# Performance work log

Hardware: AMD Instinct MI355X
Metric: run time of the kernel (lower is better)

## Reference

```python
import jax, jax.numpy as jnp
import numpy as np

N_BASE = 4          # len('NACGT'[1:])
STATE_LEN = 5
S = N_BASE ** STATE_LEN   # 1024 states
NZ = N_BASE + 1           # 5 transitions per state
T_STEPS = 800
BATCH = 32


def _build_idx():
    # idx[i] = [i, 0*256 + i//4, 1*256 + i//4, 2*256 + i//4, 3*256 + i//4]
    i = np.arange(S)
    trans = np.stack([j * (S // N_BASE) + i // N_BASE for j in range(N_BASE)], axis=1)
    idx = np.concatenate([i[:, None], trans], axis=1).astype(np.int64)      # (S, NZ)
    # transposed transition structure (stable sort: duplicates grouped deterministically)
    idx_T = np.argsort(idx.ravel(), kind='stable').reshape(S, NZ)
    idx_T_div = idx_T // NZ
    return jnp.asarray(idx), jnp.asarray(idx_T), jnp.asarray(idx_T_div)


def _scan(Ms, idx, v0):
    """Log-semiring recurrence: alpha[t+1] = logsumexp(Ms[t] + alpha[t][:, idx], -1).
    Ms: (T, N, S, NZ); idx: (S, NZ); v0: (N, S). Returns (T+1, N, S)."""
    def step(alpha, M):
        nxt = jax.scipy.special.logsumexp(M + alpha[:, idx], axis=-1)  # (N, S)
        return nxt, nxt
    _, alphas = jax.lax.scan(step, v0, Ms)
    return jnp.concatenate([v0[None], alphas], axis=0)


def setup_inputs() -> dict:
    key = jax.random.key(0)
    scores = jax.random.normal(key, (T_STEPS, BATCH, S * NZ), dtype=jnp.float32)
    return {"scores": scores}


def reference(scores):
    idx, idx_T, idx_T_div = _build_idx()
    T, N, _ = scores.shape
    Ms = scores.reshape(T, N, S, NZ)
    v0 = jnp.zeros((N, S), scores.dtype)   # semiring Log.one == 0.0
    # forward scores
    fwd = _scan(Ms, idx, v0)                                   # (T+1, N, S)
    # backward scores: gather transposed transitions, run scan in reverse time
    Ms_T = scores[:, :, idx_T]                                 # (T, N, S, NZ)
    bwd = jnp.flip(_scan(jnp.flip(Ms_T, 0), idx_T_div, v0), 0)  # (T+1, N, S)
    posts = jax.nn.softmax(fwd + bwd, axis=-1)                 # (T+1, N, S)
    return (jnp.swapaxes(scores, 0, 1),
            jnp.swapaxes(bwd, 0, 1),
            jnp.swapaxes(posts, 0, 1))
```

## Files before the change

### kernel.cpp

```cpp
#include <hip/hip_runtime.h>

#define T_STEPS 800
#define NBATCH  32
#define SST     1024
#define ROW     5120
#define STRIDE  (NBATCH * ROW)
#define NSLOT   4

__device__ __forceinline__ float lse5(float v0, float v1, float v2, float v3, float v4) {
  float m = fmaxf(fmaxf(fmaxf(v0, v1), fmaxf(v2, v3)), v4);
  float s = __expf(v0 - m) + __expf(v1 - m) + __expf(v2 - m) +
            __expf(v3 - m) + __expf(v4 - m);
  return m + __logf(s);
}

#define WAITVM(N) do { \
  asm volatile("s_waitcnt vmcnt(" #N ")" ::: "memory"); \
  __builtin_amdgcn_sched_barrier(0); } while (0)

__device__ __forceinline__ void barrier_lgkm() {
  asm volatile("s_waitcnt lgkmcnt(0)" ::: "memory");
  __builtin_amdgcn_s_barrier();
  asm volatile("" ::: "memory");
}

template <int DIR>
__device__ void loader_run(const float* __restrict__ base,
                           float* __restrict__ out0n, int l, int lane,
                           float* __restrict__ ring) {
  const int loff = 1280 * l + 4 * lane;
  const ptrdiff_t str = DIR ? -(ptrdiff_t)STRIDE : (ptrdiff_t)STRIDE;
  const float* gIss = base + (size_t)(DIR ? (T_STEPS - 1) * STRIDE : 0) + loff;
  float* ringl = ring + loff;

  float4 A0, A1, A2, A3, A4, B0, B1, B2, B3, B4, C0, C1, C2, C3, C4;

#define LOADSET(R0,R1,R2,R3,R4) do { \
    const float4* gp_ = (const float4*)gIss; \
    R0 = gp_[0]; R1 = gp_[64]; R2 = gp_[128]; R3 = gp_[192]; R4 = gp_[256]; \
    gIss += str; } while (0)

#define WRITESET(R0,R1,R2,R3,R4) do { \
    float4* lw_ = (float4*)lsWr; \
    lw_[0] = R0; lw_[64] = R1; lw_[128] = R2; lw_[192] = R3; lw_[256] = R4; \
    if constexpr (!DIR) { \
      float4* op_ = (float4*)oSt; \
      op_[0] = R0; op_[64] = R1; op_[128] = R2; op_[192] = R3; op_[256] = R4; \
      oSt += ROW; } \
    wslot = (wslot + 1) & (NSLOT - 1); \
    lsWr = ringl + wslot * ROW; } while (0)

  LOADSET(A0,A1,A2,A3,A4);
  LOADSET(B0,B1,B2,B3,B4);
  LOADSET(C0,C1,C2,C3,C4);
  int wslot = 0;
  float* lsWr = ringl;
  float* oSt = out0n + loff;
  WAITVM(10);
  WRITESET(A0,A1,A2,A3,A4);
  if constexpr (!DIR) { WAITVM(10); } else { WAITVM(5); }
  WRITESET(B0,B1,B2,B3,B4);
  barrier_lgkm();

#define LSTEP(I0,I1,I2,I3,I4, W0,W1,W2,W3,W4) do { \
    LOADSET(I0,I1,I2,I3,I4); \
    if constexpr (!DIR) { WAITVM(10); } else { WAITVM(5); } \
    WRITESET(W0,W1,W2,W3,W4); \
    barrier_lgkm(); } while (0)

  for (int c = 0; c < 265; ++c) {
    LSTEP(A0,A1,A2,A3,A4, C0,C1,C2,C3,C4);
    LSTEP(B0,B1,B2,B3,B4, A0,A1,A2,A3,A4);
    LSTEP(C0,C1,C2,C3,C4, B0,B1,B2,B3,B4);
  }
  LSTEP(A0,A1,A2,A3,A4, C0,C1,C2,C3,C4);
  LSTEP(B0,B1,B2,B3,B4, A0,A1,A2,A3,A4);
  if constexpr (!DIR) { WAITVM(5); } else { WAITVM(0); }
  WRITESET(B0,B1,B2,B3,B4);
  barrier_lgkm();
  barrier_lgkm();
  barrier_lgkm();
#undef LSTEP
#undef WRITESET
#undef LOADSET
}

template <int DIR>
__device__ void compute_run(float* __restrict__ out, int n, int u,
                            const float* __restrict__ ring, float (*abuf)[SST]) {
  float* outn = out + (size_t)n * (T_STEPS + 1) * SST;
  float a[4] = {0.f, 0.f, 0.f, 0.f};

  {
    const float4 z = {0.f, 0.f, 0.f, 0.f};
    *(float4*)&abuf[0][4 * u] = z;
    const size_t t0 = DIR ? (size_t)T_STEPS : 0;
    ((float4*)(outn + t0 * SST))[u] = z;
  }
  barrier_lgkm();

  const float* rb = ring;
  int slot = 0;
  for (int s = 0; s < T_STEPS; ++s) {
    const int cur = s & 1, nxt = cur ^ 1;
    const float4* rv = (const float4*)(rb + 20 * u);
    const float4 q0 = rv[0], q1 = rv[1], q2 = rv[2], q3 = rv[3], q4 = rv[4];
    float fv[20];
    fv[0]=q0.x; fv[1]=q0.y; fv[2]=q0.z; fv[3]=q0.w;
    fv[4]=q1.x; fv[5]=q1.y; fv[6]=q1.z; fv[7]=q1.w;
    fv[8]=q2.x; fv[9]=q2.y; fv[10]=q2.z; fv[11]=q2.w;
    fv[12]=q3.x; fv[13]=q3.y; fv[14]=q3.z; fv[15]=q3.w;
    fv[16]=q4.x; fv[17]=q4.y; fv[18]=q4.z; fv[19]=q4.w;

    float na[4];
    if constexpr (!DIR) {
      const int q = u >> 2;
      const float p0 = abuf[cur][q];
      const float p1 = abuf[cur][q + 256];
      const float p2 = abuf[cur][q + 512];
      const float p3 = abuf[cur][q + 768];
#pragma unroll
      for (int j = 0; j < 4; ++j) {
        na[j] = lse5(fv[5*j] + a[j], fv[5*j+1] + p0, fv[5*j+2] + p1,
                     fv[5*j+3] + p2, fv[5*j+4] + p3);
        a[j] = na[j];
      }
      const float4 o = {na[0], na[1], na[2], na[3]};
      ((float4*)(outn + (size_t)(s + 1) * SST))[u] = o;
      *(float4*)&abuf[nxt][4 * u] = o;
    } else {
      const float4 pv = *(const float4*)&abuf[cur][4 * u];
      const float s0 = rb[5*u], s1 = rb[5*u+1280], s2 = rb[5*u+2560], s3 = rb[5*u+3840];
      const int t = T_STEPS - 1 - s;
      na[0] = lse5(s0 + a[0], fv[1] + pv.x, fv[6] + pv.y, fv[11] + pv.z, fv[16] + pv.w);
      na[1] = lse5(s1 + a[1], fv[2] + pv.x, fv[7] + pv.y, fv[12] + pv.z, fv[17] + pv.w);
      na[2] = lse5(s2 + a[2], fv[3] + pv.x, fv[8] + pv.y, fv[13] + pv.z, fv[18] + pv.w);
      na[3] = lse5(s3 + a[3], fv[4] + pv.x, fv[9] + pv.y, fv[14] + pv.z, fv[19] + pv.w);
#pragma unroll
      for (int j = 0; j < 4; ++j) {
        a[j] = na[j];
        outn[(size_t)t * SST + u + 256 * j] = na[j];
        abuf[nxt][u + 256 * j] = na[j];
      }
    }
    barrier_lgkm();
    slot = (slot + 1) & (NSLOT - 1);
    rb = ring + slot * ROW;
  }
}

__global__ __launch_bounds__(512, 1) void mega(const float* __restrict__ scores,
                                               float* __restrict__ out0,
                                               float* __restrict__ bwdo,
                                               float* __restrict__ fposts) {
  __shared__ float ring[NSLOT * ROW];
  __shared__ float abuf[2][SST];
  const int b = blockIdx.x;
  const int tid = threadIdx.x;
  const int n = (b < NBATCH) ? b : (b - NBATCH);
  const float* base = scores + (size_t)n * ROW;

  if (b < NBATCH) {
    if (tid < 256) compute_run<0>(fposts, n, tid, ring, abuf);
    else loader_run<0>(base, out0 + (size_t)n * T_STEPS * ROW,
                       (tid >> 6) - 4, tid & 63, ring);
  } else {
    if (tid < 256) compute_run<1>(bwdo, n, tid, ring, abuf);
    else loader_run<1>(base, nullptr, (tid >> 6) - 4, tid & 63, ring);
  }
}

__global__ __launch_bounds__(256) void posts_kernel(float* __restrict__ fp,
                                                    const float* __restrict__ bp) {
  const int lane = threadIdx.x & 63;
  const int wid  = threadIdx.x >> 6;
  const size_t row = (size_t)blockIdx.x * 4 + wid;
  float* f = fp + row * SST;
  const float* b = bp + row * SST;

  float x[16];
#pragma unroll
  for (int k = 0; k < 4; ++k) {
    const float4 fv = ((const float4*)f)[lane + 64 * k];
    const float4 bv = ((const float4*)b)[lane + 64 * k];
    x[4 * k + 0] = fv.x + bv.x;
    x[4 * k + 1] = fv.y + bv.y;
    x[4 * k + 2] = fv.z + bv.z;
    x[4 * k + 3] = fv.w + bv.w;
  }
  float m = x[0];
#pragma unroll
  for (int j = 1; j < 16; ++j) m = fmaxf(m, x[j]);
#pragma unroll
  for (int off = 32; off >= 1; off >>= 1) m = fmaxf(m, __shfl_xor(m, off));
  float ssum = 0.0f;
#pragma unroll
  for (int j = 0; j < 16; ++j) { x[j] = __expf(x[j] - m); ssum += x[j]; }
#pragma unroll
  for (int off = 32; off >= 1; off >>= 1) ssum += __shfl_xor(ssum, off);
  const float inv = 1.0f / ssum;
#pragma unroll
  for (int k = 0; k < 4; ++k) {
    float4 o;
    o.x = x[4 * k + 0] * inv;
    o.y = x[4 * k + 1] * inv;
    o.z = x[4 * k + 2] * inv;
    o.w = x[4 * k + 3] * inv;
    ((float4*)f)[lane + 64 * k] = o;
  }
}

extern "C" void kernel_launch(void* const* d_in, const int* in_sizes, int n_in,
                              void* d_out, int out_size, void* d_ws, size_t ws_size,
                              hipStream_t stream) {
  (void)in_sizes; (void)n_in; (void)d_ws; (void)ws_size; (void)out_size;
  const float* scores = (const float*)d_in[0];
  float* out = (float*)d_out;
  float* out0   = out;
  float* bwdo   = out + (size_t)NBATCH * T_STEPS * ROW;
  float* fposts = bwdo + (size_t)NBATCH * (T_STEPS + 1) * SST;

  mega<<<2 * NBATCH, 512, 0, stream>>>(scores, out0, bwdo, fposts);
  posts_kernel<<<(NBATCH * (T_STEPS + 1)) / 4, 256, 0, stream>>>(fposts, bwdo);
}
```

Baseline: 737.3 us.

## Add helper blocks that prefetch score rows into cache ahead of scan blocks

Launches 192 extra workgroups alongside the forward/backward scan blocks. They stream through the score tensor in time order (96 forward from t=0, 96 backward from t=799) and do dummy reads, meant to pull data into the shared L2/MALL cache before the latency-bound loader warps need it. The result is written only under an impossible condition, so the reads are not optimised away. This costs extra HBM traffic and CU occupancy, and it only helps if the helpers stay ahead of the scan and the prefetched lines are not evicted before use.

Measured after the change: 826.0 us. +12.0%, slower.

```diff
diff --git a/kernel.cpp b/kernel.cpp
--- a/kernel.cpp
+++ b/kernel.cpp
@@ -6,6 +6,8 @@
 #define ROW     5120
 #define STRIDE  (NBATCH * ROW)
 #define NSLOT   4
+#define ARMY_F  96
+#define ARMY_B  96
 
 __device__ __forceinline__ float lse5(float v0, float v1, float v2, float v3, float v4) {
   float m = fmaxf(fmaxf(fmaxf(v0, v1), fmaxf(v2, v3)), v4);
@@ -149,24 +151,49 @@
   }
 }
 
+__device__ void army_run(const float* __restrict__ scores, int t0, int dt,
+                         float* __restrict__ ws) {
+  const int tid = threadIdx.x;
+  float acc0 = 0.f, acc1 = 0.f, acc2 = 0.f, acc3 = 0.f;
+  for (int t = t0; (unsigned)t < (unsigned)T_STEPS; t += dt) {
+    const float4* p = (const float4*)(scores + (size_t)t * STRIDE) + tid;
+#pragma unroll
+    for (int k = 0; k < 80; k += 4) {
+      const float4 a = p[(k + 0) * 512];
+      const float4 b = p[(k + 1) * 512];
+      const float4 c = p[(k + 2) * 512];
+      const float4 d = p[(k + 3) * 512];
+      acc0 += a.x; acc1 += b.x; acc2 += c.x; acc3 += d.x;
+    }
+  }
+  const float s = acc0 + acc1 + acc2 + acc3;
+  if (s == 1e38f) ws[blockIdx.x] = s;
+}
+
 __global__ __launch_bounds__(512, 1) void mega(const float* __restrict__ scores,
                                                float* __restrict__ out0,
                                                float* __restrict__ bwdo,
-                                               float* __restrict__ fposts) {
+                                               float* __restrict__ fposts,
+                                               float* __restrict__ ws) {
   __shared__ float ring[NSLOT * ROW];
   __shared__ float abuf[2][SST];
   const int b = blockIdx.x;
   const int tid = threadIdx.x;
-  const int n = (b < NBATCH) ? b : (b - NBATCH);
-  const float* base = scores + (size_t)n * ROW;
 
   if (b < NBATCH) {
-    if (tid < 256) compute_run<0>(fposts, n, tid, ring, abuf);
-    else loader_run<0>(base, out0 + (size_t)n * T_STEPS * ROW,
+    const float* base = scores + (size_t)b * ROW;
+    if (tid < 256) compute_run<0>(fposts, b, tid, ring, abuf);
+    else loader_run<0>(base, out0 + (size_t)b * T_STEPS * ROW,
                        (tid >> 6) - 4, tid & 63, ring);
-  } else {
+  } else if (b < 2 * NBATCH) {
+    const int n = b - NBATCH;
+    const float* base = scores + (size_t)n * ROW;
     if (tid < 256) compute_run<1>(bwdo, n, tid, ring, abuf);
     else loader_run<1>(base, nullptr, (tid >> 6) - 4, tid & 63, ring);
+  } else if (b < 2 * NBATCH + ARMY_F) {
+    army_run(scores, b - 2 * NBATCH, ARMY_F, ws);
+  } else {
+    army_run(scores, T_STEPS - 1 - (b - 2 * NBATCH - ARMY_F), -ARMY_B, ws);
   }
 }
 
@@ -213,13 +240,14 @@
 extern "C" void kernel_launch(void* const* d_in, const int* in_sizes, int n_in,
                               void* d_out, int out_size, void* d_ws, size_t ws_size,
                               hipStream_t stream) {
-  (void)in_sizes; (void)n_in; (void)d_ws; (void)ws_size; (void)out_size;
+  (void)in_sizes; (void)n_in; (void)ws_size; (void)out_size;
   const float* scores = (const float*)d_in[0];
   float* out = (float*)d_out;
   float* out0   = out;
   float* bwdo   = out + (size_t)NBATCH * T_STEPS * ROW;
   float* fposts = bwdo + (size_t)NBATCH * (T_STEPS + 1) * SST;
 
-  mega<<<2 * NBATCH, 512, 0, stream>>>(scores, out0, bwdo, fposts);
+  mega<<<2 * NBATCH + ARMY_F + ARMY_B, 512, 0, stream>>>(scores, out0, bwdo, fposts,
+                                                         (float*)d_ws);
   posts_kernel<<<(NBATCH * (T_STEPS + 1)) / 4, 256, 0, stream>>>(fposts, bwdo);
 }
```
